# Kernel optimization log

Measured on AMD Instinct MI355X. Metric: run time of the kernel, lower is better.

The kernel has to match this reference:

```python
import jax, jax.numpy as jnp
import numpy as np

V = 16000   # src/trg vocab
E = 512     # embedding dim (encoder_dim = decoder_dim)
H = 512     # hidden_size
L = 2       # n_layers
S = 128     # src len
T = 128     # trg len
B = 64      # batch


def _lstm_stack(x, Wih, Whh, bih, bhh, h0, c0):
    """Multi-layer LSTM, PyTorch gate order (i, f, g, o).
    x: [T, B, E]; Wih/Whh: [L, 4H, *]; bih/bhh: [L, 4H]; h0/c0: [L, B, H].
    Returns (outputs [T,B,H], hN [L,B,H], cN [L,B,H]). Dropout is eval-mode (identity)."""
    inp = x
    hs, cs = [], []
    for l in range(Wih.shape[0]):
        W1, W2 = Wih[l], Whh[l]
        b = bih[l] + bhh[l]
        def step(carry, xt, W1=W1, W2=W2, b=b):
            h, c = carry
            g = xt @ W1.T + h @ W2.T + b          # [B, 4H]
            i, f, gg, o = jnp.split(g, 4, axis=-1)
            c = jax.nn.sigmoid(f) * c + jax.nn.sigmoid(i) * jnp.tanh(gg)
            h = jax.nn.sigmoid(o) * jnp.tanh(c)
            return (h, c), h
        (h, c), ys = jax.lax.scan(step, (h0[l], c0[l]), inp)
        inp = ys
        hs.append(h)
        cs.append(c)
    return inp, jnp.stack(hs), jnp.stack(cs)


def setup_inputs() -> dict:
    key = jax.random.key(0)
    ks = jax.random.split(key, 16)
    u = lambda k, shape: jax.random.uniform(k, shape, jnp.float32, -0.08, 0.08)
    inp = {
        "src": jax.random.randint(ks[0], (S, B), 0, V),
        "trg": jax.random.randint(ks[1], (T, B), 0, V),
        "teacher_forcing_ratio": 1,
        "enc_emb": u(ks[2], (V, E)),
        "dec_emb": u(ks[3], (V, E)),
        "enc_Wih": jnp.stack([u(ks[4], (4 * H, E)), u(ks[5], (4 * H, H))]),
        "enc_Whh": u(ks[6], (L, 4 * H, H)),
        "enc_bih": u(ks[7], (L, 4 * H)),
        "enc_bhh": u(ks[8], (L, 4 * H)),
        "dec_Wih": jnp.stack([u(ks[9], (4 * H, E)), u(ks[10], (4 * H, H))]),
        "dec_Whh": u(ks[11], (L, 4 * H, H)),
        "dec_bih": u(ks[12], (L, 4 * H)),
        "dec_bhh": u(ks[13], (L, 4 * H)),
        "out_W": u(ks[14], (V, H)),
        "out_b": u(ks[15], (V,)),
    }
    return inp


def reference(src, trg, teacher_forcing_ratio, enc_emb, dec_emb,
              enc_Wih, enc_Whh, enc_bih, enc_bhh,
              dec_Wih, dec_Whh, dec_bih, dec_bhh, out_W, out_b):
    # Encoder: embed + 2-layer LSTM over src; keep final (h, c).
    zeros = jnp.zeros((L, B, H), enc_emb.dtype)
    _, h, c = _lstm_stack(enc_emb[src], enc_Wih, enc_Whh, enc_bih, enc_bhh, zeros, zeros)
    # Decoder: teacher_forcing_ratio=1 => input at step t is trg[t-1];
    # the per-step python loop collapses to one LSTM scan over trg[:-1].
    dec_in = dec_emb[trg[:-1]]                    # [T-1, B, E]
    ys, _, _ = _lstm_stack(dec_in, dec_Wih, dec_Whh, dec_bih, dec_bhh, h, c)
    logits = jnp.einsum('tbh,vh->tbv', ys, out_W) + out_b   # [T-1, B, V]
    # original: outputs[1:].view(-1, V)
    return logits.reshape(-1, V)
```

## Files before the change

### kernel.cpp

```cpp
#include <hip/hip_runtime.h>


typedef __attribute__((ext_vector_type(8))) short v8s;
typedef __attribute__((ext_vector_type(4))) short v4s;
typedef __attribute__((ext_vector_type(8))) _Float16 v8h;
typedef __attribute__((ext_vector_type(4))) float v4f;
typedef __attribute__((ext_vector_type(4))) unsigned int v4u;

#define AS1 __attribute__((address_space(1)))
#define AS3 __attribute__((address_space(3)))

__device__ __forceinline__ short f2h(float x) {
  _Float16 h = (_Float16)x;
  return __builtin_bit_cast(short, h);
}
__device__ __forceinline__ void gload16(const void* g, void* l) {
  __builtin_amdgcn_global_load_lds((const AS1 void*)g, (AS3 void*)l, 16, 0, 0);
}
__device__ __forceinline__ float sigf(float x) { return 1.f / (1.f + __expf(-x)); }
__device__ __forceinline__ float tanhfast(float x) { return 2.f / (1.f + __expf(-2.f * x)) - 1.f; }

__device__ __forceinline__ void ld16_sc1(v4u& d, const void* p) {
  asm volatile("global_load_dwordx4 %0, %1, off sc1" : "=v"(d) : "v"(p) : "memory");
}
__device__ __forceinline__ void ld16(v4u& d, const void* p) {
  asm volatile("global_load_dwordx4 %0, %1, off" : "=v"(d) : "v"(p));
}

__device__ __forceinline__ void poll32(const unsigned* flags, int base, unsigned tgt) {
  int lane = threadIdx.x & 63;
  const unsigned* fp = flags + (size_t)(base + (lane & 31)) * 16;
  while (true) {
    unsigned v;
    asm volatile("global_load_dword %0, %1, off sc1\n\ts_waitcnt vmcnt(0)"
                 : "=v"(v) : "v"(fp) : "memory");
    if (__all((int)((lane >= 32) || (v >= tgt)))) break;
    __builtin_amdgcn_s_sleep(1);
  }
}

__global__ void conv_w(const float* __restrict__ in, short* __restrict__ out,
                       int rows, int ldo, int coloff, int reorder) {
  int i = blockIdx.x * 256 + threadIdx.x;
  if (i >= rows * 128) return;
  int r = i >> 7, k4 = (i & 127) * 4;
  int rr = reorder ? (((r >> 4) & 31) * 64 + (r >> 9) * 16 + (r & 15)) : r;
  float4 v = *(const float4*)(in + (size_t)r * 512 + k4);
  v4s s; s[0] = f2h(v.x); s[1] = f2h(v.y); s[2] = f2h(v.z); s[3] = f2h(v.w);
  *(v4s*)(out + (size_t)rr * ldo + coloff + k4) = s;
}

__global__ void conv_b(const float* __restrict__ a, const float* __restrict__ b,
                       float* __restrict__ o) {
  int r = blockIdx.x * 256 + threadIdx.x;
  if (r < 2048) o[((r >> 4) & 31) * 64 + (r >> 9) * 16 + (r & 15)] = a[r] + b[r];
}

__global__ void embed_k(const int* __restrict__ ids, const float* __restrict__ emb,
                        short* __restrict__ out, int nvalid) {
  int row = blockIdx.x;
  int e = threadIdx.x * 2;
  float2 v = make_float2(0.f, 0.f);
  if (row < nvalid) {
    int id = ids[row];
    v = *(const float2*)(emb + (size_t)id * 512 + e);
  }
  unsigned pack = ((unsigned)(unsigned short)f2h(v.y) << 16) | (unsigned short)f2h(v.x);
  *(unsigned*)(out + (size_t)row * 512 + e) = pack;
}

__global__ void zero_k(short* p, int n) {
  int i = blockIdx.x * 256 + threadIdx.x;
  if (i < n) p[i] = 0;
}

#define GF_BIAS 2
#define GF_GUARDM 4

__global__ __launch_bounds__(256, 2) void gemm_bt(
    const short* __restrict__ Am, const short* __restrict__ Bm,
    const float* __restrict__ bias, float* __restrict__ Cm,
    int M, int N, int K, int ldc, int flags) {
  __shared__ short lA[128 * 64];
  __shared__ short lB[128 * 64];
  const int tid = threadIdx.x, lane = tid & 63, wave = tid >> 6;
  const int wm = wave >> 1, wn = wave & 1;
  const int tm = blockIdx.y, tn = blockIdx.x;
  v4f acc[4][4] = {};
  const short* Abase = Am + (size_t)tm * 128 * K;
  const short* Bbase = Bm + (size_t)tn * 128 * K;

  for (int kt = 0; kt < K; kt += 64) {
    __syncthreads();
#pragma unroll
    for (int i2 = 0; i2 < 4; ++i2) {
      int c = (wave * 4 + i2) * 64 + lane;
      int row = c >> 3, ch = c & 7;
      int sch = ch ^ (row & 7);
      gload16(Abase + (size_t)row * K + kt + sch * 8, (char*)lA + (wave * 4 + i2) * 1024);
      gload16(Bbase + (size_t)row * K + kt + sch * 8, (char*)lB + (wave * 4 + i2) * 1024);
    }
    asm volatile("s_waitcnt vmcnt(0)" ::: "memory");
    __syncthreads();
#pragma unroll
    for (int kc = 0; kc < 2; ++kc) {
      v8h af[4], bh[4];
#pragma unroll
      for (int mt = 0; mt < 4; ++mt) {
        int row = wm * 64 + mt * 16 + (lane & 15);
        af[mt] = *(const v8h*)((const char*)lA + row * 128 +
                               ((kc * 64 + (lane >> 4) * 16) ^ ((row & 7) << 4)));
      }
#pragma unroll
      for (int nt = 0; nt < 4; ++nt) {
        int row = wn * 64 + nt * 16 + (lane & 15);
        bh[nt] = *(const v8h*)((const char*)lB + row * 128 +
                               ((kc * 64 + (lane >> 4) * 16) ^ ((row & 7) << 4)));
      }
#pragma unroll
      for (int mt = 0; mt < 4; ++mt)
#pragma unroll
        for (int nt = 0; nt < 4; ++nt)
          acc[mt][nt] = __builtin_amdgcn_mfma_f32_16x16x32_f16(af[mt], bh[nt], acc[mt][nt], 0, 0, 0);
    }
  }

  const int rbase = tm * 128 + wm * 64 + (lane >> 4) * 4;
  const int cbase = tn * 128 + wn * 64 + (lane & 15);
#pragma unroll
  for (int mt = 0; mt < 4; ++mt) {
#pragma unroll
    for (int nt = 0; nt < 4; ++nt) {
      int gc = cbase + nt * 16;
      float bv = (flags & GF_BIAS) ? bias[gc] : 0.f;
#pragma unroll
      for (int rg = 0; rg < 4; ++rg) {
        int gr = rbase + mt * 16 + rg;
        if ((flags & GF_GUARDM) && gr >= M) continue;
        Cm[(size_t)gr * ldc + gc] = acc[mt][nt][rg] + bv;
      }
    }
  }
}

struct PipeArgs {
  const short* W0e;
  const short* W0d;
  const short* W1e;
  const short* W1d;
  const short* X;
  const float* b0e;
  const float* b0d;
  const float* b1e;
  const float* b1d;
  short* h0;
  short* h1;
  unsigned* flags;
  int Tenc, Ttot;
};

#define SLOT 32768

__global__ __launch_bounds__(256, 1) void lstm_pipe(PipeArgs A) {
  __shared__ __align__(16) short Wlds[64 * 1024];
  __shared__ __align__(16) short hsm[64 * 16];
  const int tid = threadIdx.x, lane = tid & 63, wave = tid >> 6;
  const int w = blockIdx.x, layer = w >> 5, wl = w & 31;

  auto stage = [&](const short* Wsrc) {
    for (int i = tid * 8; i < 64 * 1024; i += 256 * 8) {
      int row = i >> 10, k = i & 1023;
      v8s v = *(const v8s*)(Wsrc + (size_t)row * 1024 + k);
      *(v8s*)((char*)Wlds + row * 2048 + ((k * 2) ^ ((row & 7) << 4))) = v;
    }
  };
  stage((layer ? A.W1e : A.W0e) + (size_t)(wl * 64) * 1024);

  const int uu = lane & 15;
  float beV[4], bdV[4];
#pragma unroll
  for (int g = 0; g < 4; ++g) {
    beV[g] = (layer ? A.b1e : A.b0e)[wl * 64 + g * 16 + uu];
    bdV[g] = (layer ? A.b1d : A.b0d)[wl * 64 + g * 16 + uu];
  }
  float creg[4] = {0.f, 0.f, 0.f, 0.f};

  const int arow = wave * 16 + uu;
  const int koff = (lane >> 4) * 8;
  const size_t aoff = (size_t)arow * 512 + koff;
  __syncthreads();

  for (int t = 0; t < A.Ttot; ++t) {
    if (t == A.Tenc) {
      stage((layer ? A.W1d : A.W0d) + (size_t)(wl * 64) * 1024);
      __syncthreads();
    }

    v4f acc[4] = {};

    if (layer) {
      if (wave == 0) poll32(A.flags, 0, (unsigned)(t + 1));
      __syncthreads();
    }
    {
      const short* p1 = (layer ? (A.h0 + (size_t)(t + 1) * SLOT)
                               : (A.X + (size_t)t * SLOT)) + aoff;
      v4u fa[16];
      if (layer) {
#pragma unroll
        for (int kc = 0; kc < 16; ++kc) ld16_sc1(fa[kc], p1 + kc * 32);
      } else {
#pragma unroll
        for (int kc = 0; kc < 16; ++kc) ld16(fa[kc], p1 + kc * 32);
      }
      asm volatile("s_waitcnt vmcnt(0)" ::: "memory");
      __builtin_amdgcn_sched_barrier(0);
#pragma unroll
      for (int kc = 0; kc < 16; ++kc) {
        v8h af = __builtin_bit_cast(v8h, fa[kc]);
        int kg = kc * 32 + koff;
#pragma unroll
        for (int nt = 0; nt < 4; ++nt) {
          int wrow = nt * 16 + uu;
          v8h bh = *(const v8h*)((const char*)Wlds + wrow * 2048 +
                                 ((kg * 2) ^ ((wrow & 7) << 4)));
          acc[nt] = __builtin_amdgcn_mfma_f32_16x16x32_f16(af, bh, acc[nt], 0, 0, 0);
        }
      }
    }

    if (t > 0) {
      if (wave == 0) poll32(A.flags, layer ? 32 : 0, (unsigned)t);
      __syncthreads();
    }
    {
      const short* p2 = ((layer ? A.h1 : A.h0) + (size_t)t * SLOT) + aoff;
      v4u fb[16];
#pragma unroll
      for (int kc = 0; kc < 16; ++kc) ld16_sc1(fb[kc], p2 + kc * 32);
      asm volatile("s_waitcnt vmcnt(0)" ::: "memory");
      __builtin_amdgcn_sched_barrier(0);
#pragma unroll
      for (int kc = 0; kc < 16; ++kc) {
        v8h af = __builtin_bit_cast(v8h, fb[kc]);
        int kg = (kc + 16) * 32 + koff;
#pragma unroll
        for (int nt = 0; nt < 4; ++nt) {
          int wrow = nt * 16 + uu;
          v8h bh = *(const v8h*)((const char*)Wlds + wrow * 2048 +
                                 ((kg * 2) ^ ((wrow & 7) << 4)));
          acc[nt] = __builtin_amdgcn_mfma_f32_16x16x32_f16(af, bh, acc[nt], 0, 0, 0);
        }
      }
    }

    {
      const bool enc = t < A.Tenc;
      const float b0v = enc ? beV[0] : bdV[0];
      const float b1v = enc ? beV[1] : bdV[1];
      const float b2v = enc ? beV[2] : bdV[2];
      const float b3v = enc ? beV[3] : bdV[3];
#pragma unroll
      for (int rg = 0; rg < 4; ++rg) {
        float g0 = acc[0][rg] + b0v;
        float g1 = acc[1][rg] + b1v;
        float g2 = acc[2][rg] + b2v;
        float g3 = acc[3][rg] + b3v;
        float c = sigf(g1) * creg[rg] + sigf(g0) * tanhfast(g2);
        creg[rg] = c;
        float h = sigf(g3) * tanhfast(c);
        int bb = wave * 16 + ((lane >> 4) << 2) + rg;
        hsm[bb * 16 + uu] = f2h(h);
      }
    }
    __syncthreads();

    if (tid < 128) {
      int b = tid >> 1, half = tid & 1;
      v4u d = *(const v4u*)(&hsm[b * 16 + half * 8]);
      short* dst = (layer ? A.h1 : A.h0) + (size_t)(t + 1) * SLOT
                   + b * 512 + wl * 16 + half * 8;
      asm volatile("global_store_dwordx4 %0, %1, off sc1" :: "v"(dst), "v"(d) : "memory");
    }
    asm volatile("s_waitcnt vmcnt(0)" ::: "memory");
    __syncthreads();
    if (tid == 0) {
      unsigned val = (unsigned)(t + 1);
      const unsigned* fp = A.flags + (size_t)w * 16;
      asm volatile("global_store_dword %0, %1, off sc1" :: "v"(fp), "v"(val) : "memory");
    }
  }
}

extern "C" void kernel_launch(void* const* d_in, const int* in_sizes, int n_in,
                              void* d_out, int out_size, void* d_ws, size_t ws_size,
                              hipStream_t stream) {
  (void)in_sizes; (void)n_in; (void)out_size; (void)ws_size;
  const int* src = (const int*)d_in[0];
  const int* trg = (const int*)d_in[1];
  const float* enc_emb = (const float*)d_in[3];
  const float* dec_emb = (const float*)d_in[4];
  const float* enc_Wih = (const float*)d_in[5];
  const float* enc_Whh = (const float*)d_in[6];
  const float* enc_bih = (const float*)d_in[7];
  const float* enc_bhh = (const float*)d_in[8];
  const float* dec_Wih = (const float*)d_in[9];
  const float* dec_Whh = (const float*)d_in[10];
  const float* dec_bih = (const float*)d_in[11];
  const float* dec_bhh = (const float*)d_in[12];
  const float* out_W = (const float*)d_in[13];
  const float* out_b = (const float*)d_in[14];

  char* p = (char*)d_ws;
  auto alloc = [&](size_t sz) { char* r = p; p += (sz + 255) & ~(size_t)255; return r; };
  short* H0 = (short*)alloc((size_t)256 * SLOT * 2);
  short* H1 = (short*)alloc((size_t)257 * SLOT * 2);
  short* W0e = (short*)alloc((size_t)2048 * 1024 * 2);
  short* W0d = (short*)alloc((size_t)2048 * 1024 * 2);
  short* W1e = (short*)alloc((size_t)2048 * 1024 * 2);
  short* W1d = (short*)alloc((size_t)2048 * 1024 * 2);
  short* XO = (short*)alloc((size_t)255 * SLOT * 2);
  float* bE0 = (float*)alloc(2048 * 4);
  float* bE1 = (float*)alloc(2048 * 4);
  float* bD0 = (float*)alloc(2048 * 4);
  float* bD1 = (float*)alloc(2048 * 4);
  unsigned* flags = (unsigned*)alloc(64 * 16 * 4);

  zero_k<<<128, 256, 0, stream>>>(H0, 32768);
  zero_k<<<128, 256, 0, stream>>>(H1, 32768);
  zero_k<<<128, 256, 0, stream>>>(H1 + (size_t)256 * SLOT, 32768);
  zero_k<<<8, 256, 0, stream>>>((short*)flags, 2048);

  conv_w<<<1024, 256, 0, stream>>>(enc_Wih, W0e, 2048, 1024, 0, 1);
  conv_w<<<1024, 256, 0, stream>>>(enc_Whh, W0e, 2048, 1024, 512, 1);
  conv_w<<<1024, 256, 0, stream>>>(dec_Wih, W0d, 2048, 1024, 0, 1);
  conv_w<<<1024, 256, 0, stream>>>(dec_Whh, W0d, 2048, 1024, 512, 1);
  conv_w<<<1024, 256, 0, stream>>>(enc_Wih + (size_t)2048 * 512, W1e, 2048, 1024, 0, 1);
  conv_w<<<1024, 256, 0, stream>>>(enc_Whh + (size_t)2048 * 512, W1e, 2048, 1024, 512, 1);
  conv_w<<<1024, 256, 0, stream>>>(dec_Wih + (size_t)2048 * 512, W1d, 2048, 1024, 0, 1);
  conv_w<<<1024, 256, 0, stream>>>(dec_Whh + (size_t)2048 * 512, W1d, 2048, 1024, 512, 1);
  conv_b<<<8, 256, 0, stream>>>(enc_bih, enc_bhh, bE0);
  conv_b<<<8, 256, 0, stream>>>(enc_bih + 2048, enc_bhh + 2048, bE1);
  conv_b<<<8, 256, 0, stream>>>(dec_bih, dec_bhh, bD0);
  conv_b<<<8, 256, 0, stream>>>(dec_bih + 2048, dec_bhh + 2048, bD1);

  embed_k<<<8192, 256, 0, stream>>>(src, enc_emb, XO, 8192);
  embed_k<<<8128, 256, 0, stream>>>(trg, dec_emb, XO + (size_t)8192 * 512, 8128);

  PipeArgs pa = {W0e, W0d, W1e, W1d, XO, bE0, bD0, bE1, bD1,
                 H0, H1, flags, 128, 255};
  lstm_pipe<<<64, 256, 0, stream>>>(pa);

  short* outWb = XO;
  conv_w<<<8000, 256, 0, stream>>>(out_W, outWb, 16000, 512, 0, 0);

  gemm_bt<<<dim3(125, 64), 256, 0, stream>>>(H1 + (size_t)129 * SLOT, outWb, out_b,
                                             (float*)d_out, 8128, 16000, 512, 16000,
                                             GF_BIAS | GF_GUARDM);
}
```

Measured before the change: 2.344 ms.

## Fuse output projection GEMM into LSTM pipeline kernel via flag-gated work queue

Launches extra persistent blocks alongside the 64 LSTM blocks. They pull GEMM tiles from an atomic work queue and wait on layer-1 progress flags, so the output projection overlaps the recurrent decoder instead of running after it. Layer 1 now polls both layer-0 and its own flags once per step and loads both inputs in one batch, which removes a second sync point. This relies on co-residency of all blocks and needs extra workspace for the converted output weights, falling back to the old path when space is short.

```diff
diff --git a/kernel.cpp b/kernel.cpp
--- a/kernel.cpp
+++ b/kernel.cpp
@@ -38,6 +38,29 @@
     __builtin_amdgcn_s_sleep(1);
   }
 }
+__device__ __forceinline__ void poll_dual(const unsigned* flags, int t) {
+  int lane = threadIdx.x & 63;
+  unsigned tgt = (lane < 32) ? (unsigned)(t + 1) : (unsigned)t;
+  const unsigned* fp = flags + (size_t)lane * 16;
+  while (true) {
+    unsigned v;
+    asm volatile("global_load_dword %0, %1, off sc1\n\ts_waitcnt vmcnt(0)"
+                 : "=v"(v) : "v"(fp) : "memory");
+    if (__all((int)(v >= tgt))) break;
+    __builtin_amdgcn_s_sleep(1);
+  }
+}
+__device__ __forceinline__ void poll_l1(const unsigned* flags, unsigned thr) {
+  int lane = threadIdx.x & 63;
+  const unsigned* fp = flags + (size_t)(32 + (lane & 31)) * 16;
+  while (true) {
+    unsigned v;
+    asm volatile("global_load_dword %0, %1, off sc1\n\ts_waitcnt vmcnt(0)"
+                 : "=v"(v) : "v"(fp) : "memory");
+    if (__all((int)((lane >= 32) || (v >= thr)))) break;
+    __builtin_amdgcn_s_sleep(16);
+  }
+}
 
 __global__ void conv_w(const float* __restrict__ in, short* __restrict__ out,
                        int rows, int ldo, int coloff, int reorder) {
@@ -76,6 +99,70 @@
 
 #define GF_BIAS 2
 #define GF_GUARDM 4
+#define SLOT 32768
+
+__device__ __forceinline__ void gemm_tile(
+    const short* Abase, const short* Bbase, const float* bias, float* Cm,
+    int M, int K, int ldc, int tm, int tn, int flags,
+    short* lA, short* lB) {
+  const int tid = threadIdx.x, lane = tid & 63, wave = tid >> 6;
+  const int wm = wave >> 1, wn = wave & 1;
+  v4f acc[4][4] = {};
+  const short* At = Abase + (size_t)tm * 128 * K;
+  const short* Bt = Bbase + (size_t)tn * 128 * K;
+
+  for (int kt = 0; kt < K; kt += 64) {
+    __syncthreads();
+#pragma unroll
+    for (int i2 = 0; i2 < 4; ++i2) {
+      int c = (wave * 4 + i2) * 64 + lane;
+      int row = c >> 3, ch = c & 7;
+      int sch = ch ^ (row & 7);
+      gload16(At + (size_t)row * K + kt + sch * 8, (char*)lA + (wave * 4 + i2) * 1024);
+      gload16(Bt + (size_t)row * K + kt + sch * 8, (char*)lB + (wave * 4 + i2) * 1024);
+    }
+    asm volatile("s_waitcnt vmcnt(0)" ::: "memory");
+    __syncthreads();
+#pragma unroll
+    for (int kc = 0; kc < 2; ++kc) {
+      v8h af[4], bh[4];
+#pragma unroll
+      for (int mt = 0; mt < 4; ++mt) {
+        int row = wm * 64 + mt * 16 + (lane & 15);
+        af[mt] = *(const v8h*)((const char*)lA + row * 128 +
+                               ((kc * 64 + (lane >> 4) * 16) ^ ((row & 7) << 4)));
+      }
+#pragma unroll
+      for (int nt = 0; nt < 4; ++nt) {
+        int row = wn * 64 + nt * 16 + (lane & 15);
+        bh[nt] = *(const v8h*)((const char*)lB + row * 128 +
+                               ((kc * 64 + (lane >> 4) * 16) ^ ((row & 7) << 4)));
+      }
+#pragma unroll
+      for (int mt = 0; mt < 4; ++mt)
+#pragma unroll
+        for (int nt = 0; nt < 4; ++nt)
+          acc[mt][nt] = __builtin_amdgcn_mfma_f32_16x16x32_f16(af[mt], bh[nt], acc[mt][nt], 0, 0, 0);
+    }
+  }
+
+  const int rbase = tm * 128 + wm * 64 + (lane >> 4) * 4;
+  const int cbase = tn * 128 + wn * 64 + (lane & 15);
+#pragma unroll
+  for (int mt = 0; mt < 4; ++mt) {
+#pragma unroll
+    for (int nt = 0; nt < 4; ++nt) {
+      int gc = cbase + nt * 16;
+      float bv = (flags & GF_BIAS) ? bias[gc] : 0.f;
+#pragma unroll
+      for (int rg = 0; rg < 4; ++rg) {
+        int gr = rbase + mt * 16 + rg;
+        if ((flags & GF_GUARDM) && gr >= M) continue;
+        Cm[(size_t)gr * ldc + gc] = acc[mt][nt][rg] + bv;
+      }
+    }
+  }
+}
 
 __global__ __launch_bounds__(256, 2) void gemm_bt(
     const short* __restrict__ Am, const short* __restrict__ Bm,
@@ -83,67 +170,10 @@
     int M, int N, int K, int ldc, int flags) {
   __shared__ short lA[128 * 64];
   __shared__ short lB[128 * 64];
-  const int tid = threadIdx.x, lane = tid & 63, wave = tid >> 6;
-  const int wm = wave >> 1, wn = wave & 1;
-  const int tm = blockIdx.y, tn = blockIdx.x;
-  v4f acc[4][4] = {};
-  const short* Abase = Am + (size_t)tm * 128 * K;
-  const short* Bbase = Bm + (size_t)tn * 128 * K;
-
-  for (int kt = 0; kt < K; kt += 64) {
-    __syncthreads();
-#pragma unroll
-    for (int i2 = 0; i2 < 4; ++i2) {
-      int c = (wave * 4 + i2) * 64 + lane;
-      int row = c >> 3, ch = c & 7;
-      int sch = ch ^ (row & 7);
-      gload16(Abase + (size_t)row * K + kt + sch * 8, (char*)lA + (wave * 4 + i2) * 1024);
-      gload16(Bbase + (size_t)row * K + kt + sch * 8, (char*)lB + (wave * 4 + i2) * 1024);
-    }
-    asm volatile("s_waitcnt vmcnt(0)" ::: "memory");
-    __syncthreads();
-#pragma unroll
-    for (int kc = 0; kc < 2; ++kc) {
-      v8h af[4], bh[4];
-#pragma unroll
-      for (int mt = 0; mt < 4; ++mt) {
-        int row = wm * 64 + mt * 16 + (lane & 15);
-        af[mt] = *(const v8h*)((const char*)lA + row * 128 +
-                               ((kc * 64 + (lane >> 4) * 16) ^ ((row & 7) << 4)));
-      }
-#pragma unroll
-      for (int nt = 0; nt < 4; ++nt) {
-        int row = wn * 64 + nt * 16 + (lane & 15);
-        bh[nt] = *(const v8h*)((const char*)lB + row * 128 +
-                               ((kc * 64 + (lane >> 4) * 16) ^ ((row & 7) << 4)));
-      }
-#pragma unroll
-      for (int mt = 0; mt < 4; ++mt)
-#pragma unroll
-        for (int nt = 0; nt < 4; ++nt)
-          acc[mt][nt] = __builtin_amdgcn_mfma_f32_16x16x32_f16(af[mt], bh[nt], acc[mt][nt], 0, 0, 0);
-    }
-  }
-
-  const int rbase = tm * 128 + wm * 64 + (lane >> 4) * 4;
-  const int cbase = tn * 128 + wn * 64 + (lane & 15);
-#pragma unroll
-  for (int mt = 0; mt < 4; ++mt) {
-#pragma unroll
-    for (int nt = 0; nt < 4; ++nt) {
-      int gc = cbase + nt * 16;
-      float bv = (flags & GF_BIAS) ? bias[gc] : 0.f;
-#pragma unroll
-      for (int rg = 0; rg < 4; ++rg) {
-        int gr = rbase + mt * 16 + rg;
-        if ((flags & GF_GUARDM) && gr >= M) continue;
-        Cm[(size_t)gr * ldc + gc] = acc[mt][nt][rg] + bv;
-      }
-    }
-  }
-}
-
-struct PipeArgs {
+  gemm_tile(Am, Bm, bias, Cm, M, K, ldc, blockIdx.y, blockIdx.x, flags, lA, lB);
+}
+
+struct FusedArgs {
   const short* W0e;
   const short* W0d;
   const short* W1e;
@@ -156,16 +186,43 @@
   short* h0;
   short* h1;
   unsigned* flags;
+  unsigned* wq;
+  const short* Bgem;
+  const float* obias;
+  float* Cout;
   int Tenc, Ttot;
 };
 
-#define SLOT 32768
-
-__global__ __launch_bounds__(256, 1) void lstm_pipe(PipeArgs A) {
-  __shared__ __align__(16) short Wlds[64 * 1024];
-  __shared__ __align__(16) short hsm[64 * 16];
+__global__ __launch_bounds__(256, 1) void lstm_fused(FusedArgs A) {
+  __shared__ __align__(16) char smem[133120];
   const int tid = threadIdx.x, lane = tid & 63, wave = tid >> 6;
-  const int w = blockIdx.x, layer = w >> 5, wl = w & 31;
+  const int bid = blockIdx.x;
+
+  if (bid >= 64) {
+    short* lA = (short*)smem;
+    short* lB = (short*)(smem + 16384);
+    int* sQ = (int*)(smem + 32768);
+    while (true) {
+      if (tid == 0)
+        *sQ = (int)__hip_atomic_fetch_add(A.wq, 1u, __ATOMIC_RELAXED,
+                                          __HIP_MEMORY_SCOPE_AGENT);
+      __syncthreads();
+      int id = *sQ;
+      __syncthreads();
+      if (id >= 8000) break;
+      int tm = id / 125, tn = id - tm * 125;
+      unsigned thr = 130 + 2 * tm; if (thr > 255) thr = 255;
+      if (wave == 0) poll_l1(A.flags, thr);
+      __syncthreads();
+      gemm_tile(A.h1 + (size_t)129 * SLOT, A.Bgem, A.obias, A.Cout,
+                8128, 512, 16000, tm, tn, GF_BIAS | GF_GUARDM, lA, lB);
+    }
+    return;
+  }
+
+  short* Wlds = (short*)smem;
+  short* hsm = (short*)(smem + 131072);
+  const int w = bid, layer = w >> 5, wl = w & 31;
 
   auto stage = [&](const short* Wsrc) {
     for (int i = tid * 8; i < 64 * 1024; i += 256 * 8) {
@@ -199,25 +256,20 @@
     v4f acc[4] = {};
 
     if (layer) {
-      if (wave == 0) poll32(A.flags, 0, (unsigned)(t + 1));
+      if (wave == 0) poll_dual(A.flags, t);
       __syncthreads();
-    }
-    {
-      const short* p1 = (layer ? (A.h0 + (size_t)(t + 1) * SLOT)
-                               : (A.X + (size_t)t * SLOT)) + aoff;
-      v4u fa[16];
-      if (layer) {
-#pragma unroll
-        for (int kc = 0; kc < 16; ++kc) ld16_sc1(fa[kc], p1 + kc * 32);
-      } else {
-#pragma unroll
-        for (int kc = 0; kc < 16; ++kc) ld16(fa[kc], p1 + kc * 32);
-      }
+      const short* p1 = A.h0 + (size_t)(t + 1) * SLOT + aoff;
+      const short* p2 = A.h1 + (size_t)t * SLOT + aoff;
+      v4u fl[32];
+#pragma unroll
+      for (int kc = 0; kc < 16; ++kc) ld16_sc1(fl[kc], p1 + kc * 32);
+#pragma unroll
+      for (int kc = 0; kc < 16; ++kc) ld16_sc1(fl[16 + kc], p2 + kc * 32);
       asm volatile("s_waitcnt vmcnt(0)" ::: "memory");
       __builtin_amdgcn_sched_barrier(0);
 #pragma unroll
-      for (int kc = 0; kc < 16; ++kc) {
-        v8h af = __builtin_bit_cast(v8h, fa[kc]);
+      for (int kc = 0; kc < 32; ++kc) {
+        v8h af = __builtin_bit_cast(v8h, fl[kc]);
         int kg = kc * 32 + koff;
 #pragma unroll
         for (int nt = 0; nt < 4; ++nt) {
@@ -227,29 +279,49 @@
           acc[nt] = __builtin_amdgcn_mfma_f32_16x16x32_f16(af, bh, acc[nt], 0, 0, 0);
         }
       }
-    }
-
-    if (t > 0) {
-      if (wave == 0) poll32(A.flags, layer ? 32 : 0, (unsigned)t);
-      __syncthreads();
-    }
-    {
-      const short* p2 = ((layer ? A.h1 : A.h0) + (size_t)t * SLOT) + aoff;
-      v4u fb[16];
-#pragma unroll
-      for (int kc = 0; kc < 16; ++kc) ld16_sc1(fb[kc], p2 + kc * 32);
-      asm volatile("s_waitcnt vmcnt(0)" ::: "memory");
-      __builtin_amdgcn_sched_barrier(0);
-#pragma unroll
-      for (int kc = 0; kc < 16; ++kc) {
-        v8h af = __builtin_bit_cast(v8h, fb[kc]);
-        int kg = (kc + 16) * 32 + koff;
-#pragma unroll
-        for (int nt = 0; nt < 4; ++nt) {
-          int wrow = nt * 16 + uu;
-          v8h bh = *(const v8h*)((const char*)Wlds + wrow * 2048 +
-                                 ((kg * 2) ^ ((wrow & 7) << 4)));
-          acc[nt] = __builtin_amdgcn_mfma_f32_16x16x32_f16(af, bh, acc[nt], 0, 0, 0);
+    } else {
+      {
+        const short* p1 = A.X + (size_t)t * SLOT + aoff;
+        v4u fa[16];
+#pragma unroll
+        for (int kc = 0; kc < 16; ++kc) ld16(fa[kc], p1 + kc * 32);
+        asm volatile("s_waitcnt vmcnt(0)" ::: "memory");
+        __builtin_amdgcn_sched_barrier(0);
+#pragma unroll
+        for (int kc = 0; kc < 16; ++kc) {
+          v8h af = __builtin_bit_cast(v8h, fa[kc]);
+          int kg = kc * 32 + koff;
+#pragma unroll
+          for (int nt = 0; nt < 4; ++nt) {
+            int wrow = nt * 16 + uu;
+            v8h bh = *(const v8h*)((const char*)Wlds + wrow * 2048 +
+                                   ((kg * 2) ^ ((wrow & 7) << 4)));
+            acc[nt] = __builtin_amdgcn_mfma_f32_16x16x32_f16(af, bh, acc[nt], 0, 0, 0);
+          }
+        }
+      }
+      if (t > 0) {
+        if (wave == 0) poll32(A.flags, 0, (unsigned)t);
+        __syncthreads();
+      }
+      {
+        const short* p2 = A.h0 + (size_t)t * SLOT + aoff;
+        v4u fb[16];
+#pragma unroll
+        for (int kc = 0; kc < 16; ++kc) ld16_sc1(fb[kc], p2 + kc * 32);
+        asm volatile("s_waitcnt vmcnt(0)" ::: "memory");
+        __builtin_amdgcn_sched_barrier(0);
+#pragma unroll
+        for (int kc = 0; kc < 16; ++kc) {
+          v8h af = __builtin_bit_cast(v8h, fb[kc]);
+          int kg = (kc + 16) * 32 + koff;
+#pragma unroll
+          for (int nt = 0; nt < 4; ++nt) {
+            int wrow = nt * 16 + uu;
+            v8h bh = *(const v8h*)((const char*)Wlds + wrow * 2048 +
+                                   ((kg * 2) ^ ((wrow & 7) << 4)));
+            acc[nt] = __builtin_amdgcn_mfma_f32_16x16x32_f16(af, bh, acc[nt], 0, 0, 0);
+          }
         }
       }
     }
@@ -295,7 +367,7 @@
 extern "C" void kernel_launch(void* const* d_in, const int* in_sizes, int n_in,
                               void* d_out, int out_size, void* d_ws, size_t ws_size,
                               hipStream_t stream) {
-  (void)in_sizes; (void)n_in; (void)out_size; (void)ws_size;
+  (void)in_sizes; (void)n_in; (void)out_size;
   const int* src = (const int*)d_in[0];
   const int* trg = (const int*)d_in[1];
   const float* enc_emb = (const float*)d_in[3];
@@ -324,12 +396,17 @@
   float* bE1 = (float*)alloc(2048 * 4);
   float* bD0 = (float*)alloc(2048 * 4);
   float* bD1 = (float*)alloc(2048 * 4);
-  unsigned* flags = (unsigned*)alloc(64 * 16 * 4);
+  unsigned* flags = (unsigned*)alloc(8192);
+  unsigned* wq = flags + 1024;
+  size_t common = (size_t)(p - (char*)d_ws);
+  const size_t outWbBytes = (size_t)16000 * 512 * 2;
+  bool fused = (ws_size >= common + outWbBytes + 65536);
+  short* outWb = fused ? (short*)alloc(outWbBytes) : XO;
 
   zero_k<<<128, 256, 0, stream>>>(H0, 32768);
   zero_k<<<128, 256, 0, stream>>>(H1, 32768);
   zero_k<<<128, 256, 0, stream>>>(H1 + (size_t)256 * SLOT, 32768);
-  zero_k<<<8, 256, 0, stream>>>((short*)flags, 2048);
+  zero_k<<<16, 256, 0, stream>>>((short*)flags, 4096);
 
   conv_w<<<1024, 256, 0, stream>>>(enc_Wih, W0e, 2048, 1024, 0, 1);
   conv_w<<<1024, 256, 0, stream>>>(enc_Whh, W0e, 2048, 1024, 512, 1);
@@ -347,14 +424,17 @@
   embed_k<<<8192, 256, 0, stream>>>(src, enc_emb, XO, 8192);
   embed_k<<<8128, 256, 0, stream>>>(trg, dec_emb, XO + (size_t)8192 * 512, 8128);
 
-  PipeArgs pa = {W0e, W0d, W1e, W1d, XO, bE0, bD0, bE1, bD1,
-                 H0, H1, flags, 128, 255};
-  lstm_pipe<<<64, 256, 0, stream>>>(pa);
-
-  short* outWb = XO;
-  conv_w<<<8000, 256, 0, stream>>>(out_W, outWb, 16000, 512, 0, 0);
-
-  gemm_bt<<<dim3(125, 64), 256, 0, stream>>>(H1 + (size_t)129 * SLOT, outWb, out_b,
-                                             (float*)d_out, 8128, 16000, 512, 16000,
-                                             GF_BIAS | GF_GUARDM);
-}
+  FusedArgs fa = {W0e, W0d, W1e, W1d, XO, bE0, bD0, bE1, bD1,
+                  H0, H1, flags, wq, outWb, out_b, (float*)d_out, 128, 255};
+
+  if (fused) {
+    conv_w<<<8000, 256, 0, stream>>>(out_W, outWb, 16000, 512, 0, 0);
+    lstm_fused<<<256, 256, 0, stream>>>(fa);
+  } else {
+    lstm_fused<<<64, 256, 0, stream>>>(fa);
+    conv_w<<<8000, 256, 0, stream>>>(out_W, outWb, 16000, 512, 0, 0);
+    gemm_bt<<<dim3(125, 64), 256, 0, stream>>>(H1 + (size_t)129 * SLOT, outWb, out_b,
+                                               (float*)d_out, 8128, 16000, 512, 16000,
+                                               GF_BIAS | GF_GUARDM);
+  }
+}
```

Measured after the change: 2.552 ms. 1.09x slower.
